# Kernel tuning notes

Measured on AMD Instinct MI355X. Metric: run time of the kernel, lower is better.

The kernel has to match this reference:

```python
import jax, jax.numpy as jnp
import numpy as np

INPUT_DIM = 400
G_DIM = 3 * INPUT_DIM          # 1200, per-mention repr dim
GIJ_DIM = 9 * INPUT_DIM        # 3600, pair repr dim
HIDDEN = 150
M = 10000                      # candidate mentions
P = 2000                       # pruned mentions


def _pair_positions(P, K):
    """Static (numpy) construction of (i_pos, j_pos) into pruned_idx, matching
    the original double loop: for idx, for j in pruned_idx[max(0, idx-K):idx]."""
    I = np.repeat(np.arange(P)[:, None], K, axis=1)      # [P, K]
    Jpos = I - np.arange(K, 0, -1)[None, :]              # j = idx-K .. idx-1 (ascending)
    valid = Jpos >= 0
    return I[valid], Jpos[valid]                         # row-major => same ordering as loop


def setup_inputs() -> dict:
    key = jax.random.key(0)
    ks = jax.random.split(key, 8)
    mention_reprs = jax.random.normal(ks[0], (M, G_DIM), dtype=jnp.float32)
    pruned_idx = jnp.sort(jax.random.randint(ks[1], (P,), 0, M))
    s = 0.02
    return {
        "mention_reprs": mention_reprs,
        "pruned_idx": pruned_idx,
        "K": 50,
        "W1": jax.random.normal(ks[2], (GIJ_DIM, HIDDEN), dtype=jnp.float32) * s,
        "b1": jnp.zeros((HIDDEN,), dtype=jnp.float32),
        "W2": jax.random.normal(ks[3], (HIDDEN, HIDDEN), dtype=jnp.float32) * s,
        "b2": jnp.zeros((HIDDEN,), dtype=jnp.float32),
        "W3": jax.random.normal(ks[4], (HIDDEN, 1), dtype=jnp.float32) * s,
        "b3": jnp.zeros((1,), dtype=jnp.float32),
    }


def reference(mention_reprs, pruned_idx, K, W1, b1, W2, b2, W3, b3):
    P_ = pruned_idx.shape[0]
    i_pos, j_pos = _pair_positions(P_, int(K))           # static shapes
    g_i = mention_reprs[pruned_idx[i_pos]]               # [NP, G_DIM]
    g_j = mention_reprs[pruned_idx[j_pos]]               # [NP, G_DIM]
    pairwise = jnp.concatenate([g_i, g_j, g_i * g_j], axis=1)  # [NP, 9*input_dim]
    h = jax.nn.relu(pairwise @ W1 + b1)
    h = jax.nn.relu(h @ W2 + b2)
    return (h @ W3 + b3).squeeze(-1)                     # [NP]
```

## Files before the change

### kernel.cpp

```cpp
#include <hip/hip_runtime.h>
#include <hip/hip_bf16.h>


typedef __attribute__((ext_vector_type(8))) short short8;
typedef __attribute__((ext_vector_type(4))) float f32x4;

constexpr int DP    = 1216;
constexpr int HPAD  = 160;
constexpr int NKC   = 38;
constexpr int NKC2  = 5;
constexpr int WCH1  = 5120;
constexpr int KD    = 50;
constexpr int TI    = 5;
constexpr int PB    = TI * KD;
constexpr int NGR   = KD + TI;
constexpr int TD    = KD * (KD - 1) / 2;

constexpr int OFF_WQ0 = 0;
constexpr int OFF_WQ1 = 10240;
constexpr int OFF_WQ2 = 20480;
constexpr int OFF_GQ0 = 30720;
constexpr int OFF_GQ1 = 38912;
constexpr int OFF_GQ2 = 47104;
constexpr int OFF_TI  = 55296;
constexpr int OFF_TJ  = 55808;
constexpr int SMEM_SZ = 56320;

__device__ __forceinline__ ushort bf16_rne(float x) {
  uint u = __float_as_uint(x);
  u += 0x7FFFu + ((u >> 16) & 1u);
  return (ushort)(u >> 16);
}
__device__ __forceinline__ float bf16f(ushort h) {
  return __uint_as_float((uint)h << 16);
}
__device__ __forceinline__ f32x4 mfma16(short8 a, short8 b, f32x4 c) {
  return __builtin_amdgcn_mfma_f32_16x16x32_bf16(a, b, c, 0, 0, 0);
}
__device__ __forceinline__ void g2lds16(const void* g, void* l) {
  __builtin_amdgcn_global_load_lds(
      (const __attribute__((address_space(1))) void*)g,
      (__attribute__((address_space(3))) void*)l, 16, 0, 0);
}
__device__ __forceinline__ void stage_hi(const ushort* gs, ushort* lb,
                                         int w, int lane) {
  const char* g = (const char*)gs + w * 1024 + lane * 16;
  char* l = (char*)lb + w * 1024;
  g2lds16(g, l);
  g2lds16(g + 4096, l + 4096);
  if (w < 2) g2lds16(g + 8192, l + 8192);
}
__device__ __forceinline__ void stage_G5(const float* __restrict__ G, int gw0,
                                         int c, float* buf, int w, int lane) {
#pragma unroll
  for (int r = 0; r < 2; ++r) {
    const int slot = r * 256 + w * 64 + lane;
    int row = slot >> 3, grp = slot & 7;
    row = min(row, NGR - 1);
    const float* src =
        G + (size_t)(gw0 + row) * DP + c * 32 + ((grp ^ (row & 7)) << 2);
    g2lds16(src, (char*)buf + (r * 256 + w * 64) * 16);
  }
}
__device__ __forceinline__ short8 mulcvt8(float4 a0, float4 a1, float4 b0,
                                          float4 b1) {
  float p[8] = {a0.x * b0.x, a0.y * b0.y, a0.z * b0.z, a0.w * b0.w,
                a1.x * b1.x, a1.y * b1.y, a1.z * b1.z, a1.w * b1.w};
  uint r[4];
#pragma unroll
  for (int e = 0; e < 4; ++e) {
    __hip_bfloat162 t = __float22bfloat162_rn(make_float2(p[2 * e], p[2 * e + 1]));
    r[e] = *(uint*)&t;
  }
  uint4 h = make_uint4(r[0], r[1], r[2], r[3]);
  return *(short8*)&h;
}
__device__ __forceinline__ void split1(const float* a, short8& hi, short8& lo) {
  const float4 a0 = *(const float4*)a, a1 = *(const float4*)(a + 4);
  float p[8] = {a0.x, a0.y, a0.z, a0.w, a1.x, a1.y, a1.z, a1.w};
  uint h[4], l[4];
#pragma unroll
  for (int e = 0; e < 4; ++e) {
    uint u0 = __float_as_uint(p[2 * e]), u1 = __float_as_uint(p[2 * e + 1]);
    float r0 = p[2 * e] - __uint_as_float(u0 & 0xffff0000u);
    float r1 = p[2 * e + 1] - __uint_as_float(u1 & 0xffff0000u);
    h[e] = __builtin_amdgcn_perm(u1, u0, 0x07060302u);
    l[e] = __builtin_amdgcn_perm(__float_as_uint(r1), __float_as_uint(r0),
                                 0x07060302u);
  }
  uint4 hu = make_uint4(h[0], h[1], h[2], h[3]);
  uint4 lu = make_uint4(l[0], l[1], l[2], l[3]);
  hi = *(short8*)&hu; lo = *(short8*)&lu;
}
__device__ __forceinline__ void pair_ij(int r, int K, int NP, int& i, int& j) {
  if (r >= NP) { i = 1; j = 0; return; }
  const int T = K * (K - 1) / 2;
  if (r < T) {
    int ii = (int)((1.0f + sqrtf(1.0f + 8.0f * (float)r)) * 0.5f);
    while (ii * (ii - 1) / 2 > r) --ii;
    while ((ii + 1) * ii / 2 <= r) ++ii;
    i = ii; j = r - ii * (ii - 1) / 2;
  } else {
    const int rp = r - T, q = rp / K;
    i = K + q; j = i - K + (rp - q * K);
  }
}

__global__ void k_prep_gather(const float* __restrict__ W1,
                              const float* __restrict__ W2,
                              const float* __restrict__ M,
                              const int* __restrict__ pidx,
                              ushort* __restrict__ W1ab_hi,
                              ushort* __restrict__ W1c_hi,
                              ushort* __restrict__ W2_hi,
                              float* __restrict__ G, int P) {
  if ((int)blockIdx.x < P) {
    const int i = blockIdx.x;
    const int r = pidx[i];
    const float4* src = reinterpret_cast<const float4*>(M + (size_t)r * 1200);
    float4* dst = reinterpret_cast<float4*>(G + (size_t)i * DP);
    for (int t = threadIdx.x; t < DP / 4; t += blockDim.x)
      dst[t] = (t < 300) ? src[t] : make_float4(0.f, 0.f, 0.f, 0.f);
    return;
  }
  const int NAB = 2 * NKC * HPAD * 32;
  const int NC = NKC * HPAD * 32;
  int idx = (blockIdx.x - P) * 256 + threadIdx.x;
  if (idx < NAB) {
    int s = idx / NC, r1 = idx % NC;
    int c = r1 / (HPAD * 32), r2 = r1 % (HPAD * 32);
    int col = r2 >> 5, kk = r2 & 31;
    int k = c * 32 + kk;
    float v = (k < 1200 && col < 150) ? W1[((size_t)s * 1200 + k) * 150 + col] : 0.f;
    int i0 = (col * 32 + kk) ^ ((col & 7) << 3);
    W1ab_hi[(size_t)(s * NKC + c) * WCH1 + i0] = bf16_rne(v);
  } else if (idx < NAB + NC) {
    int r1 = idx - NAB;
    int c = r1 / (HPAD * 32), r2 = r1 % (HPAD * 32);
    int col = r2 >> 5, kk = r2 & 31;
    int k = c * 32 + kk;
    float v = (k < 1200 && col < 150)
                  ? W1[((size_t)2 * 1200 + k) * 150 + col] : 0.f;
    int i0 = (col * 32 + kk) ^ ((col & 7) << 3);
    W1c_hi[(size_t)c * WCH1 + i0] = bf16_rne(v);
  } else {
    int r1 = idx - NAB - NC;
    if (r1 < NKC2 * HPAD * 32) {
      int c = r1 / (HPAD * 32), r2 = r1 % (HPAD * 32);
      int col = r2 >> 5, kk = r2 & 31;
      int k = c * 32 + kk;
      float v = (k < 150 && col < 150) ? W2[(size_t)k * 150 + col] : 0.f;
      int i0 = (col * 32 + kk) ^ ((col & 7) << 3);
      W2_hi[(size_t)c * WCH1 + i0] = bf16_rne(v);
    }
  }
}

__global__ __launch_bounds__(256, 4) void k_precomp(
    const float* __restrict__ G, const ushort* __restrict__ W1ab_hi,
    const float* __restrict__ b1, float* __restrict__ AB, int P) {
  __shared__ __align__(16) ushort Wb[2][WCH1];
  const int tid = threadIdx.x, lane = tid & 63, w = tid >> 6;
  const int l15 = lane & 15, kb = lane >> 4;
  const int rt = w & 1, ch = w >> 1;
  const int r0 = blockIdx.x * 32;
  const int slab = blockIdx.y;
  const ushort* wsrc = W1ab_hi + (size_t)slab * NKC * WCH1;

  const int row = min(r0 + rt * 16 + l15, P - 1);
  const float* g = G + (size_t)row * DP + kb * 8;
  const int lbase = (l15 * 32 + kb * 8) ^ ((l15 & 7) << 3);

  f32x4 acc[5];
#pragma unroll
  for (int b = 0; b < 5; ++b) acc[b] = (f32x4)(0.f);

  stage_hi(wsrc, Wb[0], w, lane);
  short8 ah, al;
  split1(g, ah, al);

  for (int c = 0; c < NKC; ++c) {
    __syncthreads();
    if (c < NKC - 1)
      stage_hi(wsrc + (size_t)(c + 1) * WCH1, Wb[(c + 1) & 1], w, lane);
    const ushort* wb = Wb[c & 1];
#pragma unroll
    for (int ct = 0; ct < 5; ++ct) {
      const short8 bh = *(const short8*)&wb[(ch * 5 + ct) * 512 + lbase];
      acc[ct] = mfma16(ah, bh, acc[ct]);
      acc[ct] = mfma16(al, bh, acc[ct]);
    }
    if (c < NKC - 1) split1(g + (c + 1) * 32, ah, al);
  }
  float* outp = AB + (size_t)slab * P * HPAD;
#pragma unroll
  for (int q = 0; q < 4; ++q) {
    const int r = r0 + rt * 16 + kb * 4 + q;
    if (r < P) {
#pragma unroll
      for (int ct = 0; ct < 5; ++ct) {
        const int col = (ch * 5 + ct) * 16 + l15;
        float v = acc[ct][q];
        if (slab == 0 && col < 150) v += b1[col];
        outp[(size_t)r * HPAD + col] = v;
      }
    }
  }
}

__global__ __launch_bounds__(256, 2) void k_pair(
    const float* __restrict__ G, const ushort* __restrict__ W1c_hi,
    const ushort* __restrict__ W2_hi, const float* __restrict__ AB,
    const float* __restrict__ b2, const float* __restrict__ W3,
    const float* __restrict__ b3, ushort* __restrict__ H1,
    float* __restrict__ out, int P, int K, int NP, int ND, int wlimHead) {
  __shared__ __align__(16) char smem[SMEM_SZ];
  ushort* Wq0 = (ushort*)(smem + OFF_WQ0);
  ushort* Wq1 = (ushort*)(smem + OFF_WQ1);
  ushort* Wq2 = (ushort*)(smem + OFF_WQ2);
  float*  Gq0 = (float*)(smem + OFF_GQ0);
  float*  Gq1 = (float*)(smem + OFF_GQ1);
  float*  Gq2 = (float*)(smem + OFF_GQ2);
  int* tI = (int*)(smem + OFF_TI);
  int* tJ = (int*)(smem + OFF_TJ);

  const int tid = threadIdx.x, lane = tid & 63, w = tid >> 6;
  const int l15 = lane & 15, kb = lane >> 4;
  const int lswz = (l15 * 32 + kb * 8) ^ ((l15 & 7) << 3);
  const float* ABB = AB + (size_t)P * HPAD;

  if ((int)blockIdx.x < ND) {
    const int q8 = ND >> 3, r8 = ND & 7;
    const int xcd = blockIdx.x & 7, sidx = blockIdx.x >> 3;
    const int bid = (xcd < r8) ? xcd * (q8 + 1) + sidx
                               : r8 * (q8 + 1) + (xcd - r8) * q8 + sidx;
    const int i0 = KD + bid * TI;
    const int gw0 = i0 - KD;
    ushort* H1blk = H1 + (size_t)(TD + (size_t)bid * PB) * HPAD;

    uint sI[4], sJ[4];
#pragma unroll
    for (int rt = 0; rt < 4; ++rt) {
      const int q = min(w * 64 + rt * 16 + l15, PB - 1);
      const int li = KD + q / KD, lj = q / KD + q % KD;
      sI[rt] = li * 8 + ((2 * kb) ^ (li & 7));
      sJ[rt] = lj * 8 + ((2 * kb) ^ (lj & 7));
    }

    {
      f32x4 acc[4][10];
#pragma unroll
      for (int a = 0; a < 4; ++a)
#pragma unroll
        for (int b = 0; b < 10; ++b) acc[a][b] = (f32x4)(0.f);

      stage_G5(G, gw0, 0, Gq0, w, lane);
      stage_hi(W1c_hi, Wq0, w, lane);
      stage_G5(G, gw0, 1, Gq1, w, lane);
      stage_hi(W1c_hi + (size_t)1 * WCH1, Wq1, w, lane);
      __builtin_amdgcn_sched_barrier(0);
      asm volatile("s_waitcnt vmcnt(4)" ::: "memory");
      __builtin_amdgcn_s_barrier();
      __builtin_amdgcn_sched_barrier(0);

#define D_ITER(CI, GCUR, WCUR, GN, WN, VM)                                     \
  do {                                                                         \
    if ((CI) + 2 < NKC) {                                                      \
      stage_G5(G, gw0, (CI) + 2, (GN), w, lane);                               \
      stage_hi(W1c_hi + (size_t)((CI) + 2) * WCH1, (WN), w, lane);             \
    }                                                                          \
    __builtin_amdgcn_sched_barrier(0);                                         \
    asm volatile("s_waitcnt vmcnt(" #VM ")" ::: "memory");                     \
    __builtin_amdgcn_sched_barrier(0);                                         \
    {                                                                          \
      const float4* gp_ = (const float4*)(GCUR);                               \
      const ushort* wb_ = (WCUR);                                              \
      short8 a_[4];                                                            \
      _Pragma("unroll")                                                        \
      for (int rt = 0; rt < 4; ++rt) {                                         \
        const uint si = sI[rt], sj = sJ[rt];                                   \
        a_[rt] = mulcvt8(gp_[si], gp_[si ^ 1], gp_[sj], gp_[sj ^ 1]);          \
      }                                                                        \
      _Pragma("unroll")                                                        \
      for (int ct = 0; ct < 10; ++ct) {                                        \
        const short8 bh = *(const short8*)&wb_[ct * 512 + lswz];               \
        acc[0][ct] = mfma16(a_[0], bh, acc[0][ct]);                            \
        acc[1][ct] = mfma16(a_[1], bh, acc[1][ct]);                            \
        acc[2][ct] = mfma16(a_[2], bh, acc[2][ct]);                            \
        acc[3][ct] = mfma16(a_[3], bh, acc[3][ct]);                            \
      }                                                                        \
    }                                                                          \
    __builtin_amdgcn_s_barrier();                                              \
  } while (0)

      for (int t = 0; t < 12; ++t) {
        const int c = t * 3;
        D_ITER(c,     Gq0, Wq0, Gq2, Wq2, 4);
        D_ITER(c + 1, Gq1, Wq1, Gq0, Wq0, 4);
        D_ITER(c + 2, Gq2, Wq2, Gq1, Wq1, 4);
      }
      D_ITER(36, Gq0, Wq0, Gq2, Wq2, 0);
      D_ITER(37, Gq1, Wq1, Gq2, Wq2, 0);
#undef D_ITER

#pragma unroll
      for (int rt = 0; rt < 4; ++rt)
#pragma unroll
        for (int qq = 0; qq < 4; ++qq) {
          const int rr = w * 64 + rt * 16 + kb * 4 + qq;
          if (rr < PB) {
            const int ii = i0 + rr / KD;
            const int jj = ii - KD + rr % KD;
            const float* Ar = AB + (size_t)ii * HPAD;
            const float* Br = ABB + (size_t)jj * HPAD;
            ushort* hrow = H1blk + (size_t)rr * HPAD;
#pragma unroll
            for (int ct = 0; ct < 10; ++ct) {
              const int col = ct * 16 + l15;
              const float v = acc[rt][ct][qq] + Ar[col] + Br[col];
              hrow[col] = bf16_rne(fmaxf(v, 0.f));
            }
          }
        }
    }

    asm volatile("s_waitcnt vmcnt(0)" ::: "memory");
    const ushort* h1p[4];
#pragma unroll
    for (int rt = 0; rt < 4; ++rt) {
      const int rr = min(w * 64 + rt * 16 + l15, PB - 1);
      h1p[rt] = H1blk + (size_t)rr * HPAD + kb * 8;
    }
    float b2v[10], w3v[10];
#pragma unroll
    for (int ct = 0; ct < 10; ++ct) {
      const int col = ct * 16 + l15;
      b2v[ct] = (col < 150) ? b2[col] : 0.f;
      w3v[ct] = (col < 150) ? W3[col] : 0.f;
    }
    const float b3v = b3[0];

    f32x4 acc2[4][10];
#pragma unroll
    for (int a = 0; a < 4; ++a)
#pragma unroll
      for (int b = 0; b < 10; ++b) acc2[a][b] = (f32x4)(0.f);

    stage_hi(W2_hi, Wq0, w, lane);
    short8 a2[4];
#pragma unroll
    for (int rt = 0; rt < 4; ++rt) a2[rt] = *(const short8*)h1p[rt];

#pragma unroll
    for (int c2 = 0; c2 < NKC2; ++c2) {
      __syncthreads();
      if (c2 < NKC2 - 1)
        stage_hi(W2_hi + (size_t)(c2 + 1) * WCH1, (c2 & 1) ? Wq0 : Wq1, w, lane);
      const ushort* wb = (c2 & 1) ? Wq1 : Wq0;
#pragma unroll
      for (int ct = 0; ct < 10; ++ct) {
        const short8 bh = *(const short8*)&wb[ct * 512 + lswz];
        acc2[0][ct] = mfma16(a2[0], bh, acc2[0][ct]);
        acc2[1][ct] = mfma16(a2[1], bh, acc2[1][ct]);
        acc2[2][ct] = mfma16(a2[2], bh, acc2[2][ct]);
        acc2[3][ct] = mfma16(a2[3], bh, acc2[3][ct]);
      }
      if (c2 < NKC2 - 1) {
#pragma unroll
        for (int rt = 0; rt < 4; ++rt)
          a2[rt] = *(const short8*)(h1p[rt] + (c2 + 1) * 32);
      }
    }
#pragma unroll
    for (int rt = 0; rt < 4; ++rt)
#pragma unroll
      for (int qq = 0; qq < 4; ++qq) {
        float s = 0.f;
#pragma unroll
        for (int ct = 0; ct < 10; ++ct)
          s = fmaf(fmaxf(acc2[rt][ct][qq] + b2v[ct], 0.f), w3v[ct], s);
        s += __shfl_xor(s, 1); s += __shfl_xor(s, 2);
        s += __shfl_xor(s, 4); s += __shfl_xor(s, 8);
        if (l15 == 0) {
          const int rr = w * 64 + rt * 16 + kb * 4 + qq;
          if (rr < PB) out[TD + (size_t)bid * PB + rr] = s + b3v;
        }
      }
  } else {
    const int r0 = ((int)blockIdx.x - ND) * 128;
    const int wlim = wlimHead;
    if (tid < 128) {
      int i, j;
      pair_ij(r0 + tid, K, NP, i, j);
      tI[tid] = i; tJ[tid] = j;
    }
    stage_hi(W1c_hi, Wq0, w, lane);
    __syncthreads();

    const int rowA = w * 32 + l15, rowB = rowA + 16;
    const float* gi0 = G + (size_t)tI[rowA] * DP + kb * 8;
    const float* gj0 = G + (size_t)tJ[rowA] * DP + kb * 8;
    const float* gi1 = G + (size_t)tI[rowB] * DP + kb * 8;
    const float* gj1 = G + (size_t)tJ[rowB] * DP + kb * 8;

    {
      f32x4 acc[2][10];
#pragma unroll
      for (int a = 0; a < 2; ++a)
#pragma unroll
        for (int b = 0; b < 10; ++b) acc[a][b] = (f32x4)(0.f);

      float4 x00 = *(const float4*)gi0, x01 = *(const float4*)(gi0 + 4);
      float4 y00 = *(const float4*)gj0, y01 = *(const float4*)(gj0 + 4);
      float4 x10 = *(const float4*)gi1, x11 = *(const float4*)(gi1 + 4);
      float4 y10 = *(const float4*)gj1, y11 = *(const float4*)(gj1 + 4);

#pragma unroll 2
      for (int c = 0; c < NKC; ++c) {
        if (c) __syncthreads();
        if (c < NKC - 1)
          stage_hi(W1c_hi + (size_t)(c + 1) * WCH1, (c & 1) ? Wq0 : Wq1, w, lane);
        const short8 a0 = mulcvt8(x00, x01, y00, y01);
        const short8 a1 = mulcvt8(x10, x11, y10, y11);
        if (c < NKC - 1) {
          const int cn = c + 1;
          x00 = *(const float4*)(gi0 + cn * 32); x01 = *(const float4*)(gi0 + cn * 32 + 4);
          y00 = *(const float4*)(gj0 + cn * 32); y01 = *(const float4*)(gj0 + cn * 32 + 4);
          x10 = *(const float4*)(gi1 + cn * 32); x11 = *(const float4*)(gi1 + cn * 32 + 4);
          y10 = *(const float4*)(gj1 + cn * 32); y11 = *(const float4*)(gj1 + cn * 32 + 4);
        }
        const ushort* wb = (c & 1) ? Wq1 : Wq0;
#pragma unroll
        for (int ct = 0; ct < 10; ++ct) {
          const short8 bh = *(const short8*)&wb[ct * 512 + lswz];
          acc[0][ct] = mfma16(a0, bh, acc[0][ct]);
          acc[1][ct] = mfma16(a1, bh, acc[1][ct]);
        }
      }

#pragma unroll
      for (int rt = 0; rt < 2; ++rt)
#pragma unroll
        for (int qq = 0; qq < 4; ++qq) {
          const int rr = w * 32 + rt * 16 + kb * 4 + qq;
          const int gr = r0 + rr;
          if (gr < wlim) {
            const float* Ar = AB + (size_t)tI[rr] * HPAD;
            const float* Br = ABB + (size_t)tJ[rr] * HPAD;
            ushort* hrow = H1 + (size_t)gr * HPAD;
#pragma unroll
            for (int ct = 0; ct < 10; ++ct) {
              const int col = ct * 16 + l15;
              const float v = acc[rt][ct][qq] + Ar[col] + Br[col];
              hrow[col] = bf16_rne(fmaxf(v, 0.f));
            }
          }
        }
    }

    asm volatile("s_waitcnt vmcnt(0)" ::: "memory");
    const ushort* h1p[2];
#pragma unroll
    for (int rt = 0; rt < 2; ++rt) {
      const int gr = min(r0 + w * 32 + rt * 16 + l15, NP - 1);
      h1p[rt] = H1 + (size_t)gr * HPAD + kb * 8;
    }
    float b2v[10], w3v[10];
#pragma unroll
    for (int ct = 0; ct < 10; ++ct) {
      const int col = ct * 16 + l15;
      b2v[ct] = (col < 150) ? b2[col] : 0.f;
      w3v[ct] = (col < 150) ? W3[col] : 0.f;
    }
    const float b3v = b3[0];

    f32x4 acc2[2][10];
#pragma unroll
    for (int a = 0; a < 2; ++a)
#pragma unroll
      for (int b = 0; b < 10; ++b) acc2[a][b] = (f32x4)(0.f);

    stage_hi(W2_hi, Wq0, w, lane);
    short8 a2[2];
#pragma unroll
    for (int rt = 0; rt < 2; ++rt) a2[rt] = *(const short8*)h1p[rt];

#pragma unroll
    for (int c2 = 0; c2 < NKC2; ++c2) {
      __syncthreads();
      if (c2 < NKC2 - 1)
        stage_hi(W2_hi + (size_t)(c2 + 1) * WCH1, (c2 & 1) ? Wq0 : Wq1, w, lane);
      const ushort* wb = (c2 & 1) ? Wq1 : Wq0;
#pragma unroll
      for (int ct = 0; ct < 10; ++ct) {
        const short8 bh = *(const short8*)&wb[ct * 512 + lswz];
        acc2[0][ct] = mfma16(a2[0], bh, acc2[0][ct]);
        acc2[1][ct] = mfma16(a2[1], bh, acc2[1][ct]);
      }
      if (c2 < NKC2 - 1) {
#pragma unroll
        for (int rt = 0; rt < 2; ++rt)
          a2[rt] = *(const short8*)(h1p[rt] + (c2 + 1) * 32);
      }
    }
#pragma unroll
    for (int rt = 0; rt < 2; ++rt)
#pragma unroll
      for (int qq = 0; qq < 4; ++qq) {
        float s = 0.f;
#pragma unroll
        for (int ct = 0; ct < 10; ++ct)
          s = fmaf(fmaxf(acc2[rt][ct][qq] + b2v[ct], 0.f), w3v[ct], s);
        s += __shfl_xor(s, 1); s += __shfl_xor(s, 2);
        s += __shfl_xor(s, 4); s += __shfl_xor(s, 8);
        if (l15 == 0) {
          const int gr = r0 + w * 32 + rt * 16 + kb * 4 + qq;
          if (gr < wlim) out[gr] = s + b3v;
        }
      }
  }
}

extern "C" void kernel_launch(void* const* d_in, const int* in_sizes, int n_in,
                              void* d_out, int out_size, void* d_ws, size_t ws_size,
                              hipStream_t stream) {
  const float* M    = (const float*)d_in[0];
  const int*   pidx = (const int*)d_in[1];
  const float* W1   = (const float*)d_in[3];
  const float* b1   = (const float*)d_in[4];
  const float* W2   = (const float*)d_in[5];
  const float* b2   = (const float*)d_in[6];
  const float* W3   = (const float*)d_in[7];
  const float* b3   = (const float*)d_in[8];
  float* out = (float*)d_out;

  const int P = in_sizes[1];
  const int NP = out_size;
  int K = 50;
  for (int k = 1; k <= P; ++k) {
    const long long np = (long long)k * (k - 1) / 2 + (long long)(P - k) * k;
    if (np == (long long)NP) { K = k; break; }
  }

  float* G = (float*)d_ws;
  float* AB = G + (size_t)P * DP;
  ushort* W1ab_hi = (ushort*)(AB + (size_t)2 * P * HPAD);
  ushort* W1c_hi = W1ab_hi + (size_t)2 * NKC * WCH1;
  ushort* W2_hi = W1c_hi + (size_t)NKC * WCH1;
  ushort* H1 = W2_hi + (size_t)NKC2 * WCH1;

  const int prepN = (2 * NKC + NKC + NKC2) * HPAD * 32;
  const int prepB = (prepN + 255) / 256;
  k_prep_gather<<<P + prepB, 256, 0, stream>>>(W1, W2, M, pidx, W1ab_hi,
                                               W1c_hi, W2_hi, G, P);
  dim3 gp((P + 31) / 32, 2);
  k_precomp<<<gp, 256, 0, stream>>>(G, W1ab_hi, b1, AB, P);

  int ND = 0, wlimHead, headB;
  if (K == KD && P > KD && (P - KD) % TI == 0) {
    ND = (P - KD) / TI;
    wlimHead = TD;
    headB = (TD + 127) / 128;
  } else {
    wlimHead = NP;
    headB = (NP + 127) / 128;
  }
  k_pair<<<ND + headB, 256, 0, stream>>>(G, W1c_hi, W2_hi, AB, b2, W3, b3, H1,
                                         out, P, K, NP, ND, wlimHead);
}
```

Measured before the change: 116.2 us.

## Split each pair tile across two blocks to double grid parallelism

Each 5-row pair tile of 250 pairs is now handled by two blocks of 125 rows each, doubling the number of tile blocks. Per-wave accumulators shrink from 4 to 2 row tiles, which lowers register pressure and may raise occupancy. In exchange, the G slab and W1/W2 weight chunks are staged into shared memory twice per tile, doubling that traffic and halving MFMA reuse per staged B fragment.

```diff
diff --git a/kernel.cpp b/kernel.cpp
--- a/kernel.cpp
+++ b/kernel.cpp
@@ -13,6 +13,7 @@
 constexpr int KD    = 50;
 constexpr int TI    = 5;
 constexpr int PB    = TI * KD;
+constexpr int PBH   = 125;
 constexpr int NGR   = KD + TI;
 constexpr int TD    = KD * (KD - 1) / 2;
 
@@ -213,7 +214,7 @@
     const ushort* __restrict__ W2_hi, const float* __restrict__ AB,
     const float* __restrict__ b2, const float* __restrict__ W3,
     const float* __restrict__ b3, ushort* __restrict__ H1,
-    float* __restrict__ out, int P, int K, int NP, int ND, int wlimHead) {
+    float* __restrict__ out, int P, int K, int NP, int ND2, int wlimHead) {
   __shared__ __align__(16) char smem[SMEM_SZ];
   ushort* Wq0 = (ushort*)(smem + OFF_WQ0);
   ushort* Wq1 = (ushort*)(smem + OFF_WQ1);
@@ -229,28 +230,31 @@
   const int lswz = (l15 * 32 + kb * 8) ^ ((l15 & 7) << 3);
   const float* ABB = AB + (size_t)P * HPAD;
 
-  if ((int)blockIdx.x < ND) {
-    const int q8 = ND >> 3, r8 = ND & 7;
-    const int xcd = blockIdx.x & 7, sidx = blockIdx.x >> 3;
-    const int bid = (xcd < r8) ? xcd * (q8 + 1) + sidx
-                               : r8 * (q8 + 1) + (xcd - r8) * q8 + sidx;
-    const int i0 = KD + bid * TI;
+  if ((int)blockIdx.x < ND2) {
+    const int nt = ND2 >> 1;
+    const int t = (int)blockIdx.x >> 1, half = (int)blockIdx.x & 1;
+    const int q8 = nt >> 3, r8 = nt & 7;
+    const int xcd = t & 7, sidx = t >> 3;
+    const int tile = (xcd < r8) ? xcd * (q8 + 1) + sidx
+                                : r8 * (q8 + 1) + (xcd - r8) * q8 + sidx;
+    const int i0 = KD + tile * TI;
     const int gw0 = i0 - KD;
-    ushort* H1blk = H1 + (size_t)(TD + (size_t)bid * PB) * HPAD;
-
-    uint sI[4], sJ[4];
-#pragma unroll
-    for (int rt = 0; rt < 4; ++rt) {
-      const int q = min(w * 64 + rt * 16 + l15, PB - 1);
+    const int rbase = half * PBH;
+    ushort* H1blk = H1 + (size_t)(TD + (size_t)tile * PB + rbase) * HPAD;
+
+    uint sI[2], sJ[2];
+#pragma unroll
+    for (int rt = 0; rt < 2; ++rt) {
+      const int q = min(rbase + w * 32 + rt * 16 + l15, PB - 1);
       const int li = KD + q / KD, lj = q / KD + q % KD;
       sI[rt] = li * 8 + ((2 * kb) ^ (li & 7));
       sJ[rt] = lj * 8 + ((2 * kb) ^ (lj & 7));
     }
 
     {
-      f32x4 acc[4][10];
-#pragma unroll
-      for (int a = 0; a < 4; ++a)
+      f32x4 acc[2][10];
+#pragma unroll
+      for (int a = 0; a < 2; ++a)
 #pragma unroll
         for (int b = 0; b < 10; ++b) acc[a][b] = (f32x4)(0.f);
 
@@ -275,9 +279,9 @@
     {                                                                          \
       const float4* gp_ = (const float4*)(GCUR);                               \
       const ushort* wb_ = (WCUR);                                              \
-      short8 a_[4];                                                            \
+      short8 a_[2];                                                            \
       _Pragma("unroll")                                                        \
-      for (int rt = 0; rt < 4; ++rt) {                                         \
+      for (int rt = 0; rt < 2; ++rt) {                                         \
         const uint si = sI[rt], sj = sJ[rt];                                   \
         a_[rt] = mulcvt8(gp_[si], gp_[si ^ 1], gp_[sj], gp_[sj ^ 1]);          \
       }                                                                        \
@@ -286,15 +290,13 @@
         const short8 bh = *(const short8*)&wb_[ct * 512 + lswz];               \
         acc[0][ct] = mfma16(a_[0], bh, acc[0][ct]);                            \
         acc[1][ct] = mfma16(a_[1], bh, acc[1][ct]);                            \
-        acc[2][ct] = mfma16(a_[2], bh, acc[2][ct]);                            \
-        acc[3][ct] = mfma16(a_[3], bh, acc[3][ct]);                            \
       }                                                                        \
     }                                                                          \
     __builtin_amdgcn_s_barrier();                                              \
   } while (0)
 
-      for (int t = 0; t < 12; ++t) {
-        const int c = t * 3;
+      for (int t2 = 0; t2 < 12; ++t2) {
+        const int c = t2 * 3;
         D_ITER(c,     Gq0, Wq0, Gq2, Wq2, 4);
         D_ITER(c + 1, Gq1, Wq1, Gq0, Wq0, 4);
         D_ITER(c + 2, Gq2, Wq2, Gq1, Wq1, 4);
@@ -304,16 +306,17 @@
 #undef D_ITER
 
 #pragma unroll
-      for (int rt = 0; rt < 4; ++rt)
+      for (int rt = 0; rt < 2; ++rt)
 #pragma unroll
         for (int qq = 0; qq < 4; ++qq) {
-          const int rr = w * 64 + rt * 16 + kb * 4 + qq;
-          if (rr < PB) {
+          const int lr = w * 32 + rt * 16 + kb * 4 + qq;
+          if (lr < PBH) {
+            const int rr = rbase + lr;
             const int ii = i0 + rr / KD;
             const int jj = ii - KD + rr % KD;
             const float* Ar = AB + (size_t)ii * HPAD;
             const float* Br = ABB + (size_t)jj * HPAD;
-            ushort* hrow = H1blk + (size_t)rr * HPAD;
+            ushort* hrow = H1blk + (size_t)lr * HPAD;
 #pragma unroll
             for (int ct = 0; ct < 10; ++ct) {
               const int col = ct * 16 + l15;
@@ -325,11 +328,11 @@
     }
 
     asm volatile("s_waitcnt vmcnt(0)" ::: "memory");
-    const ushort* h1p[4];
-#pragma unroll
-    for (int rt = 0; rt < 4; ++rt) {
-      const int rr = min(w * 64 + rt * 16 + l15, PB - 1);
-      h1p[rt] = H1blk + (size_t)rr * HPAD + kb * 8;
+    const ushort* h1p[2];
+#pragma unroll
+    for (int rt = 0; rt < 2; ++rt) {
+      const int lr = min(w * 32 + rt * 16 + l15, PBH - 1);
+      h1p[rt] = H1blk + (size_t)lr * HPAD + kb * 8;
     }
     float b2v[10], w3v[10];
 #pragma unroll
@@ -340,16 +343,16 @@
     }
     const float b3v = b3[0];
 
-    f32x4 acc2[4][10];
-#pragma unroll
-    for (int a = 0; a < 4; ++a)
+    f32x4 acc2[2][10];
+#pragma unroll
+    for (int a = 0; a < 2; ++a)
 #pragma unroll
       for (int b = 0; b < 10; ++b) acc2[a][b] = (f32x4)(0.f);
 
     stage_hi(W2_hi, Wq0, w, lane);
-    short8 a2[4];
-#pragma unroll
-    for (int rt = 0; rt < 4; ++rt) a2[rt] = *(const short8*)h1p[rt];
+    short8 a2[2];
+#pragma unroll
+    for (int rt = 0; rt < 2; ++rt) a2[rt] = *(const short8*)h1p[rt];
 
 #pragma unroll
     for (int c2 = 0; c2 < NKC2; ++c2) {
@@ -362,17 +365,15 @@
         const short8 bh = *(const short8*)&wb[ct * 512 + lswz];
         acc2[0][ct] = mfma16(a2[0], bh, acc2[0][ct]);
         acc2[1][ct] = mfma16(a2[1], bh, acc2[1][ct]);
-        acc2[2][ct] = mfma16(a2[2], bh, acc2[2][ct]);
-        acc2[3][ct] = mfma16(a2[3], bh, acc2[3][ct]);
       }
       if (c2 < NKC2 - 1) {
 #pragma unroll
-        for (int rt = 0; rt < 4; ++rt)
+        for (int rt = 0; rt < 2; ++rt)
           a2[rt] = *(const short8*)(h1p[rt] + (c2 + 1) * 32);
       }
     }
 #pragma unroll
-    for (int rt = 0; rt < 4; ++rt)
+    for (int rt = 0; rt < 2; ++rt)
 #pragma unroll
       for (int qq = 0; qq < 4; ++qq) {
         float s = 0.f;
@@ -382,12 +383,13 @@
         s += __shfl_xor(s, 1); s += __shfl_xor(s, 2);
         s += __shfl_xor(s, 4); s += __shfl_xor(s, 8);
         if (l15 == 0) {
-          const int rr = w * 64 + rt * 16 + kb * 4 + qq;
-          if (rr < PB) out[TD + (size_t)bid * PB + rr] = s + b3v;
+          const int lr = w * 32 + rt * 16 + kb * 4 + qq;
+          if (lr < PBH)
+            out[TD + (size_t)tile * PB + rbase + lr] = s + b3v;
         }
       }
   } else {
-    const int r0 = ((int)blockIdx.x - ND) * 128;
+    const int r0 = ((int)blockIdx.x - ND2) * 128;
     const int wlim = wlimHead;
     if (tid < 128) {
       int i, j;
@@ -556,15 +558,15 @@
   dim3 gp((P + 31) / 32, 2);
   k_precomp<<<gp, 256, 0, stream>>>(G, W1ab_hi, b1, AB, P);
 
-  int ND = 0, wlimHead, headB;
+  int ND2 = 0, wlimHead, headB;
   if (K == KD && P > KD && (P - KD) % TI == 0) {
-    ND = (P - KD) / TI;
+    ND2 = 2 * ((P - KD) / TI);
     wlimHead = TD;
     headB = (TD + 127) / 128;
   } else {
     wlimHead = NP;
     headB = (NP + 127) / 128;
   }
-  k_pair<<<ND + headB, 256, 0, stream>>>(G, W1c_hi, W2_hi, AB, b2, W3, b3, H1,
-                                         out, P, K, NP, ND, wlimHead);
-}
+  k_pair<<<ND2 + headB, 256, 0, stream>>>(G, W1c_hi, W2_hi, AB, b2, W3, b3, H1,
+                                          out, P, K, NP, ND2, wlimHead);
+}
```

New measurement: 144.7 us. 24.5% more time.
